# Kernel optimization log

Hardware: AMD Instinct MI355X
Metric: run time of the kernel (lower is better)

Reference implementation:

```python
import jax, jax.numpy as jnp
import numpy as np

B, T, D = 64, 4096, 256
UNITS = 256

def setup_inputs() -> dict:
    key = jax.random.key(0)
    k0, k1, k2, k3 = jax.random.split(key, 4)
    lstm_output = jax.random.normal(k0, (B, T, D), dtype=jnp.float32)
    # Glorot-ish scaled dense weights (no bias per module)
    W1 = jax.random.normal(k1, (D, UNITS), dtype=jnp.float32) * (1.0 / np.sqrt(D))
    W2 = jax.random.normal(k2, (D, UNITS), dtype=jnp.float32) * (1.0 / np.sqrt(D))
    v = jax.random.normal(k3, (UNITS, 1), dtype=jnp.float32) * (1.0 / np.sqrt(UNITS))
    return {"lstm_output": lstm_output, "W1": W1, "W2": W2, "v": v}

def reference(lstm_output, W1, W2, v):
    # query/key: [B, T, units]
    query = jnp.einsum("btd,du->btu", lstm_output, W1)
    key = jnp.einsum("btd,du->btu", lstm_output, W2)
    # score: [B, T, 1]
    score = jnp.einsum("btu,uo->bto", jnp.tanh(query + key), v)
    # softmax over time axis (axis=1)
    attention_weights = jax.nn.softmax(score, axis=1)
    # context: [B, D]
    context_vector = jnp.sum(attention_weights * lstm_output, axis=1)
    return (context_vector, attention_weights)
```

## Files before the change

kernel.cpp:

```cpp
#include <hip/hip_runtime.h>
#include <math.h>

#define B 64
#define T 4096
#define D 256
#define U 256

typedef __attribute__((ext_vector_type(8)))  short s16x8;
typedef __attribute__((ext_vector_type(16))) float f32x16;

#define MT 32
#define SPB 32
#define NBLK ((B*T)/(MT*SPB))
#define LDAP 33

#define TCH 256
#define NCH (T / TCH)

__global__ __launch_bounds__(512, 2) void scores_mfma_kernel(
    const float* __restrict__ A,
    const float* __restrict__ W1,
    const float* __restrict__ W2,
    const float* __restrict__ v,
    float* __restrict__ s_out)
{
  __shared__ uint4 AH[32 * LDAP];
  __shared__ uint4 AL[32 * LDAP];
  __shared__ float red[32][8];

  const int tid  = threadIdx.x;
  const int lane = tid & 63;
  const int wv   = tid >> 6;
  const int l31  = lane & 31;
  const int half = lane >> 5;

  const int n = wv * 32 + l31;
  s16x8 Bh[16], Bl[16];
#pragma unroll
  for (int s = 0; s < 16; ++s) {
    s16x8 bh, bl;
#pragma unroll
    for (int j = 0; j < 8; ++j) {
      const int k = s * 16 + half * 8 + j;
      const float w = W1[k * 256 + n] + W2[k * 256 + n];
      const unsigned int uw = __float_as_uint(w);
      const float wl = w - __uint_as_float(uw & 0xffff0000u);
      bh[j] = (short)(uw >> 16);
      bl[j] = (short)(__float_as_uint(wl) >> 16);
    }
    Bh[s] = bh; Bl[s] = bl;
  }
  const float vv = v[n];

  const int sm  = tid >> 4;
  const int sc0 = tid & 15;

  const size_t row0 = (size_t)blockIdx.x * (MT * SPB);
  float4 rg[4];
  {
    const float4* src = (const float4*)(A + (row0 + sm) * 256);
#pragma unroll
    for (int i = 0; i < 4; ++i) rg[i] = src[sc0 + 16 * i];
  }

  for (int step = 0; step < SPB; ++step) {
    const size_t rowbase = row0 + (size_t)step * MT;

#pragma unroll
    for (int i = 0; i < 4; ++i) {
      const float4 a = rg[i];
      const int k  = 4 * (sc0 + 16 * i);
      const int k8 = k >> 3;
      const int off = (k >> 2) & 1;
      const unsigned int ux = __float_as_uint(a.x), uy = __float_as_uint(a.y);
      const unsigned int uz = __float_as_uint(a.z), uw = __float_as_uint(a.w);
      const uint2 hi2 = make_uint2((ux >> 16) | (uy & 0xffff0000u),
                                   (uz >> 16) | (uw & 0xffff0000u));
      const float lx = a.x - __uint_as_float(ux & 0xffff0000u);
      const float ly = a.y - __uint_as_float(uy & 0xffff0000u);
      const float lz = a.z - __uint_as_float(uz & 0xffff0000u);
      const float lw = a.w - __uint_as_float(uw & 0xffff0000u);
      const uint2 lo2 = make_uint2(
          (__float_as_uint(lx) >> 16) | (__float_as_uint(ly) & 0xffff0000u),
          (__float_as_uint(lz) >> 16) | (__float_as_uint(lw) & 0xffff0000u));
      ((uint2*)&AH[k8 * LDAP + sm])[off] = hi2;
      ((uint2*)&AL[k8 * LDAP + sm])[off] = lo2;
    }
    __syncthreads();

    if (step + 1 < SPB) {
      const float4* src = (const float4*)(A + (rowbase + MT + sm) * 256);
#pragma unroll
      for (int i = 0; i < 4; ++i) rg[i] = src[sc0 + 16 * i];
    }

    f32x16 a0 = {}, a1 = {}, a2 = {};
#pragma unroll
    for (int s = 0; s < 16; ++s) {
      const uint4 qh = AH[(2 * s + half) * LDAP + l31];
      const uint4 ql = AL[(2 * s + half) * LDAP + l31];
      const s16x8 ah = __builtin_bit_cast(s16x8, qh);
      const s16x8 al = __builtin_bit_cast(s16x8, ql);
      a0 = __builtin_amdgcn_mfma_f32_32x32x16_bf16(ah, Bh[s], a0, 0, 0, 0);
      a1 = __builtin_amdgcn_mfma_f32_32x32x16_bf16(ah, Bl[s], a1, 0, 0, 0);
      a2 = __builtin_amdgcn_mfma_f32_32x32x16_bf16(al, Bh[s], a2, 0, 0, 0);
    }

#pragma unroll
    for (int r = 0; r < 16; ++r) {
      const float x = a0[r] + a1[r] + a2[r];
      const float e = __expf(x + x);
      const float t = 1.f - 2.f * __builtin_amdgcn_rcpf(e + 1.f);
      float p = t * vv;
      p += __shfl_xor(p, 1);
      p += __shfl_xor(p, 2);
      p += __shfl_xor(p, 4);
      p += __shfl_xor(p, 8);
      p += __shfl_xor(p, 16);
      if (l31 == 0)
        red[(r & 3) + 8 * (r >> 2) + 4 * half][wv] = p;
    }
    __syncthreads();

    if (tid < 32) {
      const float4* rp = (const float4*)&red[tid][0];
      const float4 ra = rp[0], rb = rp[1];
      s_out[rowbase + tid] = ra.x + ra.y + ra.z + ra.w + rb.x + rb.y + rb.z + rb.w;
    }
  }
}

__global__ __launch_bounds__(1024) void softmax_kernel(float* __restrict__ attn) {
    const int b = blockIdx.x;
    float* row = attn + (long)b * T;
    const int tid = threadIdx.x;
    const int wave = tid >> 6, lane = tid & 63;

    __shared__ float lmax[16];
    __shared__ float lsum[16];
    __shared__ float bcast[2];

    float4 s = ((const float4*)row)[tid];
    float m = fmaxf(fmaxf(s.x, s.y), fmaxf(s.z, s.w));
    for (int off = 32; off > 0; off >>= 1) m = fmaxf(m, __shfl_down(m, off));
    if (lane == 0) lmax[wave] = m;
    __syncthreads();
    if (tid == 0) {
        float mm = lmax[0];
        for (int i = 1; i < 16; ++i) mm = fmaxf(mm, lmax[i]);
        bcast[0] = mm;
    }
    __syncthreads();
    m = bcast[0];

    float4 e;
    e.x = expf(s.x - m); e.y = expf(s.y - m);
    e.z = expf(s.z - m); e.w = expf(s.w - m);
    float sum = e.x + e.y + e.z + e.w;
    for (int off = 32; off > 0; off >>= 1) sum += __shfl_down(sum, off);
    if (lane == 0) lsum[wave] = sum;
    __syncthreads();
    if (tid == 0) {
        float ss = 0.f;
        for (int i = 0; i < 16; ++i) ss += lsum[i];
        bcast[1] = 1.0f / ss;
    }
    __syncthreads();
    const float inv = bcast[1];
    e.x *= inv; e.y *= inv; e.z *= inv; e.w *= inv;
    ((float4*)row)[tid] = e;
}

__global__ __launch_bounds__(256) void context_partial_kernel(
    const float* __restrict__ A, const float* __restrict__ attn,
    float* __restrict__ part)
{
    const int chunk = blockIdx.x;
    const int b = blockIdx.y;
    const int tg = threadIdx.x >> 6;
    const int l = threadIdx.x & 63;
    const int dl = l * 4;
    const long tokbase = (long)b * T + (long)chunk * TCH;

    float4 acc = make_float4(0.f, 0.f, 0.f, 0.f);
    for (int t = tg; t < TCH; t += 4) {
        const long tok = tokbase + t;
        const float a = attn[tok];
        const float4 x = *(const float4*)(A + tok * D + dl);
        acc.x = fmaf(a, x.x, acc.x);
        acc.y = fmaf(a, x.y, acc.y);
        acc.z = fmaf(a, x.z, acc.z);
        acc.w = fmaf(a, x.w, acc.w);
    }

    __shared__ float4 red[4][64];
    red[tg][l] = acc;
    __syncthreads();
    if (tg == 0) {
        float4 r = red[0][l];
        const float4 r1 = red[1][l], r2 = red[2][l], r3 = red[3][l];
        r.x += r1.x + r2.x + r3.x;
        r.y += r1.y + r2.y + r3.y;
        r.z += r1.z + r2.z + r3.z;
        r.w += r1.w + r2.w + r3.w;
        float* p = part + ((long)chunk * B + b) * D + dl;
        p[0] = r.x; p[1] = r.y; p[2] = r.z; p[3] = r.w;
    }
}

__global__ void context_reduce_kernel(const float* __restrict__ part,
                                      float* __restrict__ ctx) {
    const int i = blockIdx.x * 256 + threadIdx.x;
    float s = 0.f;
    for (int c = 0; c < NCH; ++c) s += part[(long)c * (B * D) + i];
    ctx[i] = s;
}

extern "C" void kernel_launch(void* const* d_in, const int* in_sizes, int n_in,
                              void* d_out, int out_size, void* d_ws, size_t ws_size,
                              hipStream_t stream) {
    const float* lstm = (const float*)d_in[0];
    const float* W1   = (const float*)d_in[1];
    const float* W2   = (const float*)d_in[2];
    const float* v    = (const float*)d_in[3];

    float* out  = (float*)d_out;
    float* ctx  = out;
    float* attn = out + B * D;

    float* part = (float*)d_ws;

    scores_mfma_kernel<<<NBLK, 512, 0, stream>>>(lstm, W1, W2, v, attn);
    softmax_kernel<<<B, 1024, 0, stream>>>(attn);
    context_partial_kernel<<<dim3(NCH, B), 256, 0, stream>>>(lstm, attn, part);
    context_reduce_kernel<<<(B * D) / 256, 256, 0, stream>>>(part, ctx);
}
```

Before: 484.6 us.

## Use DPP row reduction, halve work per block, unroll context loads

Replaces the shuffle-xor reduction in the score epilogue with DPP adds plus a ds_swizzle, avoiding LDS-backed shuffles. Halves steps per block in the score kernel (more blocks) and the time chunk in the context kernel (more blocks, each thread handling 32 contiguous tokens with fully unrolled loads and vector weight loads). It aims to increase parallelism and memory-level parallelism, at the cost of reloading weights into registers more often per token and more partial sums to reduce.

Result: faster. 443.9 us (-8.4%).

```diff
diff --git a/kernel.cpp b/kernel.cpp
--- a/kernel.cpp
+++ b/kernel.cpp
@@ -10,12 +10,16 @@
 typedef __attribute__((ext_vector_type(16))) float f32x16;
 
 #define MT 32
-#define SPB 32
+#define SPB 16
 #define NBLK ((B*T)/(MT*SPB))
 #define LDAP 33
 
-#define TCH 256
+#define TCH 128
 #define NCH (T / TCH)
+
+#define DPP_ADD(v, ctrl)                                                     \
+  v += __int_as_float(__builtin_amdgcn_update_dpp(                           \
+      0, __float_as_int(v), ctrl, 0xF, 0xF, true))
 
 __global__ __launch_bounds__(512, 2) void scores_mfma_kernel(
     const float* __restrict__ A,
@@ -110,13 +114,13 @@
     for (int r = 0; r < 16; ++r) {
       const float x = a0[r] + a1[r] + a2[r];
       const float e = __expf(x + x);
-      const float t = 1.f - 2.f * __builtin_amdgcn_rcpf(e + 1.f);
-      float p = t * vv;
-      p += __shfl_xor(p, 1);
-      p += __shfl_xor(p, 2);
-      p += __shfl_xor(p, 4);
-      p += __shfl_xor(p, 8);
-      p += __shfl_xor(p, 16);
+      float p = (1.f - 2.f * __builtin_amdgcn_rcpf(e + 1.f)) * vv;
+      DPP_ADD(p, 0xB1);
+      DPP_ADD(p, 0x4E);
+      DPP_ADD(p, 0x141);
+      DPP_ADD(p, 0x140);
+      p += __int_as_float(
+          __builtin_amdgcn_ds_swizzle(__float_as_int(p), 0x401F));
       if (l31 == 0)
         red[(r & 3) + 8 * (r >> 2) + 4 * half][wv] = p;
     }
@@ -171,7 +175,7 @@
     ((float4*)row)[tid] = e;
 }
 
-__global__ __launch_bounds__(256) void context_partial_kernel(
+__global__ __launch_bounds__(256, 4) void context_partial_kernel(
     const float* __restrict__ A, const float* __restrict__ attn,
     float* __restrict__ part)
 {
@@ -180,17 +184,25 @@
     const int tg = threadIdx.x >> 6;
     const int l = threadIdx.x & 63;
     const int dl = l * 4;
-    const long tokbase = (long)b * T + (long)chunk * TCH;
-
+    const long tokbase = (long)b * T + (long)chunk * TCH + (long)tg * 32;
+
+    const float4* wp = (const float4*)(attn + tokbase);
     float4 acc = make_float4(0.f, 0.f, 0.f, 0.f);
-    for (int t = tg; t < TCH; t += 4) {
-        const long tok = tokbase + t;
-        const float a = attn[tok];
-        const float4 x = *(const float4*)(A + tok * D + dl);
-        acc.x = fmaf(a, x.x, acc.x);
-        acc.y = fmaf(a, x.y, acc.y);
-        acc.z = fmaf(a, x.z, acc.z);
-        acc.w = fmaf(a, x.w, acc.w);
+#pragma unroll
+    for (int t8 = 0; t8 < 32; t8 += 8) {
+        const float4 wa = wp[t8 / 4];
+        const float4 wb = wp[t8 / 4 + 1];
+        float w[8];
+        *(float4*)&w[0] = wa;
+        *(float4*)&w[4] = wb;
+#pragma unroll
+        for (int j = 0; j < 8; ++j) {
+            const float4 x = *(const float4*)(A + (tokbase + t8 + j) * 256 + dl);
+            acc.x = fmaf(w[j], x.x, acc.x);
+            acc.y = fmaf(w[j], x.y, acc.y);
+            acc.z = fmaf(w[j], x.z, acc.z);
+            acc.w = fmaf(w[j], x.w, acc.w);
+        }
     }
 
     __shared__ float4 red[4][64];
```
